# Performance work log

Hardware: AMD Instinct MI355X
Metric: run time of the kernel (lower is better)

## Reference

```python
import jax, jax.numpy as jnp
import numpy as np

DIM = 256
N_EMBED = 2048
EPS_LOG = 1e-07


def setup_inputs() -> dict:
    key = jax.random.key(0)
    k_in, k_emb = jax.random.split(key)
    inp = jax.random.normal(k_in, (16, 64, 64, DIM), dtype=jnp.float32)
    # embeddings_initial_variance = 1 -> plain randn
    embed = jax.random.normal(k_emb, (DIM, N_EMBED), dtype=jnp.float32)
    return {"input": inp, "embed": embed}


def reference(input, embed):
    # Eval-mode forward of Quantize (no EMA buffer updates).
    flatten = input.reshape(-1, DIM)                      # [N, dim]
    # squared euclidean distance via expansion:
    dist = (
        jnp.sum(flatten * flatten, axis=1, keepdims=True)
        - 2.0 * (flatten @ embed)
        + jnp.sum(embed * embed, axis=0, keepdims=True)
    )
    embed_ind_flat = jnp.argmax(-dist, axis=1)            # [N] int
    embed_ind = embed_ind_flat.reshape(input.shape[:-1])  # [B,H,W]

    # gather codes: F.embedding(embed_ind, embed.T)
    quantize = jnp.take(embed.T, embed_ind, axis=0)       # [B,H,W,dim]

    # commitment loss with detached quantize
    diff = jnp.mean((jax.lax.stop_gradient(quantize) - input) ** 2)

    # straight-through estimator
    quantize_st = input + jax.lax.stop_gradient(quantize - input)

    # perplexity from average code assignment probabilities
    n = flatten.shape[0]
    counts = jnp.zeros((N_EMBED,), dtype=flatten.dtype).at[embed_ind_flat].add(1.0)
    avg_probas = counts / n
    perplexity = jnp.exp(
        -jnp.sum(avg_probas * jnp.log(jnp.clip(avg_probas, EPS_LOG, None)))
    )
    return quantize_st, diff, embed_ind, perplexity
```

## Files before the change

### kernel.cpp

```cpp
#include <hip/hip_runtime.h>
#include <cstdint>
#include <cstddef>

#define DIM    256
#define NE     2048
#define NROWS  65536

#define OFF_DIFF ((size_t)16777216)
#define OFF_IND  ((size_t)16777217)
#define OFF_PERP ((size_t)16842753)

#define WS_DIFF   0
#define WS_CNT    64
#define WS_EN     8256
#define WS_ENC    16448
#define WS_ET     24640
#define WS_BPK    2121792
#define WS_NEED_V2 ((size_t)(2121792 + 2097152))

typedef __attribute__((ext_vector_type(8)))  _Float16 half8;
typedef __attribute__((ext_vector_type(16))) float    float16v;

__device__ __forceinline__ float16v mfma32(half8 a, half8 b, float16v c) {
    return __builtin_amdgcn_mfma_f32_32x32x16_f16(a, b, c, 0, 0, 0);
}

__device__ __forceinline__ void gld16(const void* g, void* l) {
    __builtin_amdgcn_global_load_lds((const __attribute__((address_space(1))) void*)g,
                                     (__attribute__((address_space(3))) void*)l,
                                     16, 0, 0);
}


__global__ __launch_bounds__(256) void k_prep(const float* __restrict__ embed,
                                              float* __restrict__ enorm,
                                              float* __restrict__ enc) {
    int j = blockIdx.x * 256 + threadIdx.x;
    double s = 0.0;
    for (int d = 0; d < DIM; ++d) {
        float e = embed[(size_t)d * NE + j];
        s += (double)e * (double)e;
    }
    float en = (float)s;
    enorm[j] = en;
    enc[j]   = (128.0f - 0.5f * en) * 2048.0f;
}

__global__ __launch_bounds__(256) void k_pack(const float* __restrict__ embed,
                                              _Float16* __restrict__ bpk,
                                              float* __restrict__ embedT) {
    int tt    = blockIdx.x * 256 + threadIdx.x;
    int nc    = tt >> 10;
    int tfrag = (tt >> 6) & 15;
    int lane  = tt & 63;
    int col   = nc * 32 + (lane & 31);
    int k0    = tfrag * 16 + (lane >> 5) * 8;
    half8 h, l;
#pragma unroll
    for (int j = 0; j < 8; ++j) {
        float e = embed[(size_t)(k0 + j) * NE + col];
        _Float16 eh = (_Float16)e;
        h[j] = eh;
        l[j] = (_Float16)(e - (float)eh);
        embedT[(size_t)col * DIM + k0 + j] = e;
    }
    char* base = (char*)bpk + (size_t)nc * 32768 + (size_t)tfrag * 1024 + (size_t)lane * 16;
    *(half8*)(base)         = h;
    *(half8*)(base + 16384) = l;
}


__global__ __launch_bounds__(256, 2) void k_gemm(
    const float* __restrict__ inp,
    const _Float16* __restrict__ bpk,
    const float* __restrict__ enorm,
    const float* __restrict__ enc,
    const float* __restrict__ embedT,
    float* __restrict__ out,
    int* __restrict__ counts,
    double* __restrict__ diffacc)
{
    __shared__ __align__(16) char ldsB[2][32768];
    __shared__ float encs[NE];
    const int tid  = threadIdx.x;
    const int w    = tid >> 6;
    const int lane = tid & 63;
    const int kh   = lane >> 5;
    const int m    = lane & 31;
    const int mw   = blockIdx.x * 128 + w * 32;

#pragma unroll
    for (int i = 0; i < 8; ++i) encs[tid + 256 * i] = enc[tid + 256 * i];

    half8 ah[16], al[16];
    {
        const float* xr = inp + (size_t)(mw + m) * DIM + kh * 8;
#pragma unroll
        for (int t = 0; t < 16; ++t) {
            float4 f0 = *(const float4*)(xr + t * 16);
            float4 f1 = *(const float4*)(xr + t * 16 + 4);
            float fs[8] = {f0.x, f0.y, f0.z, f0.w, f1.x, f1.y, f1.z, f1.w};
            half8 hh, ll;
#pragma unroll
            for (int j = 0; j < 8; ++j) {
                _Float16 xh = (_Float16)fs[j];
                hh[j] = xh;
                ll[j] = (_Float16)(fs[j] - (float)xh);
            }
            ah[t] = hh;
            al[t] = ll;
        }
    }

    int P1[16], P2[16];
#pragma unroll
    for (int r = 0; r < 16; ++r) { P1[r] = (int)0x80000000; P2[r] = (int)0x80000000; }

    {
        const char* src = (const char*)bpk;
#pragma unroll
        for (int s = 0; s < 8; ++s) {
            int seg = w * 8 + s;
            gld16(src + seg * 1024 + lane * 16, &ldsB[0][0] + seg * 1024);
        }
    }
    __syncthreads();

    for (int nc = 0; nc < 64; ++nc) {
        int pn = nc & 1;
        if (nc < 63) {
            const char* src = (const char*)bpk + (size_t)(nc + 1) * 32768;
            char* dst = &ldsB[pn ^ 1][0];
#pragma unroll
            for (int s = 0; s < 8; ++s) {
                int seg = w * 8 + s;
                gld16(src + seg * 1024 + lane * 16, dst + seg * 1024);
            }
        }

        float en = encs[nc * 32 + m];
        const char* bb = &ldsB[pn][0] + lane * 16;

        float16v acc = {};
#pragma unroll
        for (int t = 0; t < 16; ++t) {
            half8 bh = *(const half8*)(bb + t * 1024);
            half8 bl = *(const half8*)(bb + 16384 + t * 1024);
            acc = mfma32(ah[t], bh, acc);
            acc = mfma32(al[t], bh, acc);
            acc = mfma32(ah[t], bl, acc);
        }

        int colp = nc * 32 + m;
#pragma unroll
        for (int r = 0; r < 16; ++r) {
            float sf = fmaf(acc[r], 2048.0f, en);
            sf = __builtin_amdgcn_fmed3f(sf, -1048064.0f, 1048064.0f);
            int si = (int)sf;
            int p  = (int)(((unsigned)si << 11) | (unsigned)colp);
            int mn = (P1[r] < p) ? P1[r] : p;
            P2[r]  = (P2[r] > mn) ? P2[r] : mn;
            P1[r]  = (P1[r] > p) ? P1[r] : p;
        }
        __syncthreads();
    }

#pragma unroll
    for (int r = 0; r < 16; ++r) {
        int p1 = P1[r], p2 = P2[r];
#pragma unroll
        for (int msk = 1; msk < 32; msk <<= 1) {
            int o1 = __shfl_xor(p1, msk);
            int o2 = __shfl_xor(p2, msk);
            int mx2 = (p2 > o2) ? p2 : o2;
            int mn1 = (p1 < o1) ? p1 : o1;
            p2 = (mx2 > mn1) ? mx2 : mn1;
            p1 = (p1 > o1) ? p1 : o1;
        }
        P1[r] = p1; P2[r] = p2;
    }

    double dsum = 0.0;
#pragma unroll
    for (int rr = 0; rr < 32; ++rr) {
        const int reg = (rr & 3) | (((rr >> 3) & 3) << 2);
        const int src = ((rr >> 2) & 1) << 5;
        int i1 = __shfl(P1[reg], src) & 2047;
        int i2 = __shfl(P2[reg], src) & 2047;
        int row = mw + rr;
        float4 xv = *(const float4*)(inp    + (size_t)row * DIM + lane * 4);
        float4 e1 = *(const float4*)(embedT + (size_t)i1  * DIM + lane * 4);
        float4 e2 = *(const float4*)(embedT + (size_t)i2  * DIM + lane * 4);
        float d1 = xv.x * e1.x + xv.y * e1.y + xv.z * e1.z + xv.w * e1.w;
        float d2 = xv.x * e2.x + xv.y * e2.y + xv.z * e2.z + xv.w * e2.w;
#pragma unroll
        for (int msk = 1; msk < 64; msk <<= 1) {
            d1 += __shfl_xor(d1, msk);
            d2 += __shfl_xor(d2, msk);
        }
        float s1 = 2.f * d1 - enorm[i1];
        float s2 = 2.f * d2 - enorm[i2];
        bool take2 = (s2 > s1) || (s2 == s1 && i2 < i1);
        int win = take2 ? i2 : i1;
        float4 qv = take2 ? e2 : e1;
        *(float4*)(out + (size_t)row * DIM + lane * 4) = qv;
        float dx = qv.x - xv.x, dy = qv.y - xv.y;
        float dz = qv.z - xv.z, dw = qv.w - xv.w;
        dsum += (double)(dx * dx + dy * dy + dz * dz + dw * dw);
        if (lane == 0) {
            out[OFF_IND + row] = (float)win;
            atomicAdd(&counts[win], 1);
        }
    }
#pragma unroll
    for (int msk = 1; msk < 64; msk <<= 1) dsum += __shfl_xor(dsum, msk);
    if (lane == 0) atomicAdd(diffacc, dsum);
}

__global__ __launch_bounds__(256) void k_main(const float* __restrict__ inp,
                                              const float* __restrict__ embed,
                                              const float* __restrict__ enorm,
                                              float* __restrict__ out,
                                              int* __restrict__ counts,
                                              double* __restrict__ diffacc) {
    __shared__ float XsT[DIM][64];
    const int tid = threadIdx.x;
    const int m0  = blockIdx.x * 64;
#pragma unroll
    for (int i = 0; i < 16; ++i) {
        int f = tid + 256 * i;
        int row = f >> 6, c4 = f & 63;
        float4 v = *(const float4*)&inp[(size_t)(m0 + row) * DIM + c4 * 4];
        XsT[c4 * 4 + 0][row] = v.x; XsT[c4 * 4 + 1][row] = v.y;
        XsT[c4 * 4 + 2][row] = v.z; XsT[c4 * 4 + 3][row] = v.w;
    }
    __syncthreads();
    const int tx = tid & 15, ty = tid >> 4;
    float bv[4]; int bi[4];
#pragma unroll
    for (int mi = 0; mi < 4; ++mi) { bv[mi] = -1e30f; bi[mi] = 0x7fffffff; }
    for (int n0 = 0; n0 < NE; n0 += 64) {
        float acc[4][4] = {};
        const float* bp = embed + n0 + tx * 4;
        const float* ap = &XsT[0][ty * 4];
#pragma unroll 8
        for (int k = 0; k < DIM; ++k) {
            float4 b4 = *(const float4*)(bp + (size_t)k * NE);
            float4 a4 = *(const float4*)(ap + k * 64);
            acc[0][0] = fmaf(a4.x, b4.x, acc[0][0]); acc[0][1] = fmaf(a4.x, b4.y, acc[0][1]);
            acc[0][2] = fmaf(a4.x, b4.z, acc[0][2]); acc[0][3] = fmaf(a4.x, b4.w, acc[0][3]);
            acc[1][0] = fmaf(a4.y, b4.x, acc[1][0]); acc[1][1] = fmaf(a4.y, b4.y, acc[1][1]);
            acc[1][2] = fmaf(a4.y, b4.z, acc[1][2]); acc[1][3] = fmaf(a4.y, b4.w, acc[1][3]);
            acc[2][0] = fmaf(a4.z, b4.x, acc[2][0]); acc[2][1] = fmaf(a4.z, b4.y, acc[2][1]);
            acc[2][2] = fmaf(a4.z, b4.z, acc[2][2]); acc[2][3] = fmaf(a4.z, b4.w, acc[2][3]);
            acc[3][0] = fmaf(a4.w, b4.x, acc[3][0]); acc[3][1] = fmaf(a4.w, b4.y, acc[3][1]);
            acc[3][2] = fmaf(a4.w, b4.z, acc[3][2]); acc[3][3] = fmaf(a4.w, b4.w, acc[3][3]);
        }
        float4 en4 = *(const float4*)&enorm[n0 + tx * 4];
        int c0 = n0 + tx * 4;
#pragma unroll
        for (int mi = 0; mi < 4; ++mi) {
            float s0 = 2.f * acc[mi][0] - en4.x, s1 = 2.f * acc[mi][1] - en4.y;
            float s2 = 2.f * acc[mi][2] - en4.z, s3 = 2.f * acc[mi][3] - en4.w;
            float v = s0; int idx = c0;
            if (s1 > v) { v = s1; idx = c0 + 1; }
            if (s2 > v) { v = s2; idx = c0 + 2; }
            if (s3 > v) { v = s3; idx = c0 + 3; }
#pragma unroll
            for (int o = 1; o < 16; o <<= 1) {
                float ov = __shfl_xor(v, o, 64); int oi = __shfl_xor(idx, o, 64);
                if (ov > v || (ov == v && oi < idx)) { v = ov; idx = oi; }
            }
            if (v > bv[mi] || (v == bv[mi] && idx < bi[mi])) { bv[mi] = v; bi[mi] = idx; }
        }
    }
    __syncthreads();
    int* sidx = (int*)&XsT[0][0];
    if (tx == 0) {
#pragma unroll
        for (int mi = 0; mi < 4; ++mi) {
            int rl = ty * 4 + mi; int idx = bi[mi];
            sidx[rl] = idx;
            out[OFF_IND + m0 + rl] = (float)idx;
            atomicAdd(&counts[idx], 1);
        }
    }
    __syncthreads();
    float dsum = 0.f;
    for (int rl = 0; rl < 64; ++rl) {
        int idx = sidx[rl];
        float qv = embed[(size_t)tid * NE + idx];
        float x = inp[(size_t)(m0 + rl) * DIM + tid];
        out[(size_t)(m0 + rl) * DIM + tid] = qv;
        float d = qv - x;
        dsum = fmaf(d, d, dsum);
    }
    double ds = (double)dsum;
#pragma unroll
    for (int o = 32; o > 0; o >>= 1) ds += __shfl_down(ds, o, 64);
    double* red = (double*)&XsT[4][0];
    if ((tid & 63) == 0) red[tid >> 6] = ds;
    __syncthreads();
    if (tid == 0) atomicAdd(diffacc, red[0] + red[1] + red[2] + red[3]);
}

__global__ __launch_bounds__(256) void k_fin(const int* __restrict__ counts,
                                             const double* __restrict__ diffacc,
                                             float* __restrict__ out) {
    __shared__ double red[4];
    int tid = threadIdx.x;
    double s = 0.0;
    for (int i = tid; i < NE; i += 256) {
        int c = counts[i];
        if (c > 0) {
            float p = (float)c * (1.0f / 65536.0f);
            s += (double)(p * logf(p));
        }
    }
#pragma unroll
    for (int o = 32; o > 0; o >>= 1) s += __shfl_down(s, o, 64);
    if ((tid & 63) == 0) red[tid >> 6] = s;
    __syncthreads();
    if (tid == 0) {
        double t = red[0] + red[1] + red[2] + red[3];
        out[OFF_PERP] = expf((float)(-t));
        out[OFF_DIFF] = (float)(diffacc[0] * (1.0 / 16777216.0));
    }
}

extern "C" void kernel_launch(void* const* d_in, const int* in_sizes, int n_in,
                              void* d_out, int out_size, void* d_ws, size_t ws_size,
                              hipStream_t stream) {
    (void)in_sizes; (void)n_in; (void)out_size;
    const float* inp   = (const float*)d_in[0];
    const float* embed = (const float*)d_in[1];
    float* out = (float*)d_out;
    char*  ws  = (char*)d_ws;

    double*   diffacc = (double*)(ws + WS_DIFF);
    int*      counts  = (int*)(ws + WS_CNT);
    float*    enorm   = (float*)(ws + WS_EN);
    float*    enc     = (float*)(ws + WS_ENC);
    float*    embedT  = (float*)(ws + WS_ET);
    _Float16* bpk     = (_Float16*)(ws + WS_BPK);

    hipMemsetAsync(d_ws, 0, 8256, stream);
    k_prep<<<NE / 256, 256, 0, stream>>>(embed, enorm, enc);

    if (ws_size >= WS_NEED_V2) {
        k_pack<<<256, 256, 0, stream>>>(embed, bpk, embedT);
        k_gemm<<<NROWS / 128, 256, 0, stream>>>(inp, bpk, enorm, enc, embedT,
                                                out, counts, diffacc);
    } else {
        k_main<<<NROWS / 64, 256, 0, stream>>>(inp, embed, enorm,
                                               out, counts, diffacc);
    }
    k_fin<<<1, 256, 0, stream>>>(counts, diffacc, out);
}
```

Measured before the change: 335.3 us.

## Drop low-half embedding term, flag near-tie rows and recheck them in fp32

```diff
diff --git a/kernel.cpp b/kernel.cpp
--- a/kernel.cpp
+++ b/kernel.cpp
@@ -11,12 +11,13 @@
 #define OFF_PERP ((size_t)16842753)
 
 #define WS_DIFF   0
+#define WS_NFLAG  8
 #define WS_CNT    64
 #define WS_EN     8256
-#define WS_ENC    16448
-#define WS_ET     24640
-#define WS_BPK    2121792
-#define WS_NEED_V2 ((size_t)(2121792 + 2097152))
+#define WS_FLAG   16448
+#define WS_ET     32832
+#define WS_BPH    2129984
+#define FLAG_CAP  4096
 
 typedef __attribute__((ext_vector_type(8)))  _Float16 half8;
 typedef __attribute__((ext_vector_type(16))) float    float16v;
@@ -31,23 +32,30 @@
                                      16, 0, 0);
 }
 
-
 __global__ __launch_bounds__(256) void k_prep(const float* __restrict__ embed,
-                                              float* __restrict__ enorm,
-                                              float* __restrict__ enc) {
-    int j = blockIdx.x * 256 + threadIdx.x;
+                                              float* __restrict__ enorm) {
+    __shared__ double red[256];
+    const int tid = threadIdx.x;
+    const int cl  = tid & 31, seg = tid >> 5;
+    const int col = blockIdx.x * 32 + cl;
     double s = 0.0;
-    for (int d = 0; d < DIM; ++d) {
-        float e = embed[(size_t)d * NE + j];
+#pragma unroll 8
+    for (int k = seg * 32; k < seg * 32 + 32; ++k) {
+        float e = embed[(size_t)k * NE + col];
         s += (double)e * (double)e;
     }
-    float en = (float)s;
-    enorm[j] = en;
-    enc[j]   = (128.0f - 0.5f * en) * 2048.0f;
+    red[tid] = s;
+    __syncthreads();
+    if (seg == 0) {
+        double t = 0.0;
+#pragma unroll
+        for (int h = 0; h < 8; ++h) t += red[cl + 32 * h];
+        enorm[col] = (float)t;
+    }
 }
 
 __global__ __launch_bounds__(256) void k_pack(const float* __restrict__ embed,
-                                              _Float16* __restrict__ bpk,
+                                              _Float16* __restrict__ bph,
                                               float* __restrict__ embedT) {
     int tt    = blockIdx.x * 256 + threadIdx.x;
     int nc    = tt >> 10;
@@ -55,46 +63,37 @@
     int lane  = tt & 63;
     int col   = nc * 32 + (lane & 31);
     int k0    = tfrag * 16 + (lane >> 5) * 8;
-    half8 h, l;
+    half8 h;
 #pragma unroll
     for (int j = 0; j < 8; ++j) {
         float e = embed[(size_t)(k0 + j) * NE + col];
-        _Float16 eh = (_Float16)e;
-        h[j] = eh;
-        l[j] = (_Float16)(e - (float)eh);
+        h[j] = (_Float16)e;
         embedT[(size_t)col * DIM + k0 + j] = e;
     }
-    char* base = (char*)bpk + (size_t)nc * 32768 + (size_t)tfrag * 1024 + (size_t)lane * 16;
-    *(half8*)(base)         = h;
-    *(half8*)(base + 16384) = l;
-}
-
+    *(half8*)((char*)bph + (size_t)nc * 16384 + (size_t)tfrag * 1024 + (size_t)lane * 16) = h;
+}
 
 __global__ __launch_bounds__(256, 2) void k_gemm(
     const float* __restrict__ inp,
-    const _Float16* __restrict__ bpk,
+    const _Float16* __restrict__ bph,
     const float* __restrict__ enorm,
-    const float* __restrict__ enc,
     const float* __restrict__ embedT,
     float* __restrict__ out,
     int* __restrict__ counts,
-    double* __restrict__ diffacc)
+    double* __restrict__ diffacc,
+    int* __restrict__ nflag,
+    int* __restrict__ flags)
 {
-    __shared__ __align__(16) char ldsB[2][32768];
-    __shared__ float encs[NE];
+    __shared__ __align__(16) char ldsB[2][16384];
     const int tid  = threadIdx.x;
     const int w    = tid >> 6;
     const int lane = tid & 63;
-    const int kh   = lane >> 5;
     const int m    = lane & 31;
     const int mw   = blockIdx.x * 128 + w * 32;
 
-#pragma unroll
-    for (int i = 0; i < 8; ++i) encs[tid + 256 * i] = enc[tid + 256 * i];
-
     half8 ah[16], al[16];
     {
-        const float* xr = inp + (size_t)(mw + m) * DIM + kh * 8;
+        const float* xr = inp + (size_t)(mw + m) * DIM + (lane >> 5) * 8;
 #pragma unroll
         for (int t = 0; t < 16; ++t) {
             float4 f0 = *(const float4*)(xr + t * 16);
@@ -116,45 +115,40 @@
 #pragma unroll
     for (int r = 0; r < 16; ++r) { P1[r] = (int)0x80000000; P2[r] = (int)0x80000000; }
 
-    {
-        const char* src = (const char*)bpk;
-#pragma unroll
-        for (int s = 0; s < 8; ++s) {
-            int seg = w * 8 + s;
-            gld16(src + seg * 1024 + lane * 16, &ldsB[0][0] + seg * 1024);
-        }
+#pragma unroll
+    for (int s = 0; s < 4; ++s) {
+        int seg = w * 4 + s;
+        gld16((const char*)bph + seg * 1024 + lane * 16, &ldsB[0][0] + seg * 1024);
     }
     __syncthreads();
 
     for (int nc = 0; nc < 64; ++nc) {
         int pn = nc & 1;
         if (nc < 63) {
-            const char* src = (const char*)bpk + (size_t)(nc + 1) * 32768;
+            const char* src = (const char*)bph + (size_t)(nc + 1) * 16384;
             char* dst = &ldsB[pn ^ 1][0];
 #pragma unroll
-            for (int s = 0; s < 8; ++s) {
-                int seg = w * 8 + s;
+            for (int s = 0; s < 4; ++s) {
+                int seg = w * 4 + s;
                 gld16(src + seg * 1024 + lane * 16, dst + seg * 1024);
             }
         }
 
-        float en = encs[nc * 32 + m];
         const char* bb = &ldsB[pn][0] + lane * 16;
-
-        float16v acc = {};
+        float16v accA = {}, accB = {};
 #pragma unroll
         for (int t = 0; t < 16; ++t) {
             half8 bh = *(const half8*)(bb + t * 1024);
-            half8 bl = *(const half8*)(bb + 16384 + t * 1024);
-            acc = mfma32(ah[t], bh, acc);
-            acc = mfma32(al[t], bh, acc);
-            acc = mfma32(ah[t], bl, acc);
-        }
-
-        int colp = nc * 32 + m;
+            accA = mfma32(ah[t], bh, accA);
+            accB = mfma32(al[t], bh, accB);
+        }
+
+        float en  = enorm[nc * 32 + m];
+        float enc = fmaf(en, -1024.0f, 262144.0f);
+        int colp  = nc * 32 + m;
 #pragma unroll
         for (int r = 0; r < 16; ++r) {
-            float sf = fmaf(acc[r], 2048.0f, en);
+            float sf = fmaf(accA[r] + accB[r], 2048.0f, enc);
             sf = __builtin_amdgcn_fmed3f(sf, -1048064.0f, 1048064.0f);
             int si = (int)sf;
             int p  = (int)(((unsigned)si << 11) | (unsigned)colp);
@@ -185,8 +179,11 @@
     for (int rr = 0; rr < 32; ++rr) {
         const int reg = (rr & 3) | (((rr >> 3) & 3) << 2);
         const int src = ((rr >> 2) & 1) << 5;
-        int i1 = __shfl(P1[reg], src) & 2047;
-        int i2 = __shfl(P2[reg], src) & 2047;
+        int p1row = __shfl(P1[reg], src);
+        int p2row = __shfl(P2[reg], src);
+        int i1 = p1row & 2047;
+        int i2 = p2row & 2047;
+        float v2a = (float)(p2row >> 11) * (1.0f / 1024.0f) - 256.0f;
         int row = mw + rr;
         float4 xv = *(const float4*)(inp    + (size_t)row * DIM + lane * 4);
         float4 e1 = *(const float4*)(embedT + (size_t)i1  * DIM + lane * 4);
@@ -202,6 +199,7 @@
         float s2 = 2.f * d2 - enorm[i2];
         bool take2 = (s2 > s1) || (s2 == s1 && i2 < i1);
         int win = take2 ? i2 : i1;
+        float sW = take2 ? s2 : s1;
         float4 qv = take2 ? e2 : e1;
         *(float4*)(out + (size_t)row * DIM + lane * 4) = qv;
         float dx = qv.x - xv.x, dy = qv.y - xv.y;
@@ -210,6 +208,10 @@
         if (lane == 0) {
             out[OFF_IND + row] = (float)win;
             atomicAdd(&counts[win], 1);
+            if (sW - v2a < 0.15f) {
+                int fi = atomicAdd(nflag, 1);
+                if (fi < FLAG_CAP) flags[fi] = row;
+            }
         }
     }
 #pragma unroll
@@ -217,91 +219,119 @@
     if (lane == 0) atomicAdd(diffacc, dsum);
 }
 
-__global__ __launch_bounds__(256) void k_main(const float* __restrict__ inp,
-                                              const float* __restrict__ embed,
-                                              const float* __restrict__ enorm,
-                                              float* __restrict__ out,
-                                              int* __restrict__ counts,
-                                              double* __restrict__ diffacc) {
+__global__ __launch_bounds__(256) void k_clean(
+    const float* __restrict__ inp,
+    const float* __restrict__ embed,
+    const float* __restrict__ embedT,
+    const float* __restrict__ enorm,
+    float* __restrict__ out,
+    int* __restrict__ counts,
+    double* __restrict__ diffacc,
+    const int* __restrict__ nflagp,
+    const int* __restrict__ flags)
+{
     __shared__ float XsT[DIM][64];
+    __shared__ int rowsS[64];
+    __shared__ int newS[64];
+    __shared__ double redS[4];
+    int nf = *nflagp; if (nf > FLAG_CAP) nf = FLAG_CAP;
     const int tid = threadIdx.x;
-    const int m0  = blockIdx.x * 64;
-#pragma unroll
-    for (int i = 0; i < 16; ++i) {
-        int f = tid + 256 * i;
-        int row = f >> 6, c4 = f & 63;
-        float4 v = *(const float4*)&inp[(size_t)(m0 + row) * DIM + c4 * 4];
-        XsT[c4 * 4 + 0][row] = v.x; XsT[c4 * 4 + 1][row] = v.y;
-        XsT[c4 * 4 + 2][row] = v.z; XsT[c4 * 4 + 3][row] = v.w;
-    }
-    __syncthreads();
-    const int tx = tid & 15, ty = tid >> 4;
-    float bv[4]; int bi[4];
-#pragma unroll
-    for (int mi = 0; mi < 4; ++mi) { bv[mi] = -1e30f; bi[mi] = 0x7fffffff; }
-    for (int n0 = 0; n0 < NE; n0 += 64) {
-        float acc[4][4] = {};
-        const float* bp = embed + n0 + tx * 4;
-        const float* ap = &XsT[0][ty * 4];
+
+    for (int chunk = blockIdx.x; chunk * 64 < nf; chunk += gridDim.x) {
+        int cnt = nf - chunk * 64; if (cnt > 64) cnt = 64;
+        if (tid < 64) {
+            rowsS[tid] = flags[chunk * 64 + (tid < cnt ? tid : 0)];
+            newS[tid] = -1;
+        }
+        __syncthreads();
+#pragma unroll
+        for (int i = 0; i < 16; ++i) {
+            int f = tid + 256 * i;
+            int r = f >> 6, c4 = f & 63;
+            float4 v = *(const float4*)&inp[(size_t)rowsS[r] * DIM + c4 * 4];
+            XsT[c4 * 4 + 0][r] = v.x; XsT[c4 * 4 + 1][r] = v.y;
+            XsT[c4 * 4 + 2][r] = v.z; XsT[c4 * 4 + 3][r] = v.w;
+        }
+        __syncthreads();
+
+        const int tx = tid & 15, ty = tid >> 4;
+        float bv[4]; int bi[4];
+#pragma unroll
+        for (int mi = 0; mi < 4; ++mi) { bv[mi] = -1e30f; bi[mi] = 0x7fffffff; }
+        for (int n0 = 0; n0 < NE; n0 += 64) {
+            float acc[4][4] = {};
+            const float* bp = embed + n0 + tx * 4;
+            const float* ap = &XsT[0][ty * 4];
 #pragma unroll 8
-        for (int k = 0; k < DIM; ++k) {
-            float4 b4 = *(const float4*)(bp + (size_t)k * NE);
-            float4 a4 = *(const float4*)(ap + k * 64);
-            acc[0][0] = fmaf(a4.x, b4.x, acc[0][0]); acc[0][1] = fmaf(a4.x, b4.y, acc[0][1]);
-            acc[0][2] = fmaf(a4.x, b4.z, acc[0][2]); acc[0][3] = fmaf(a4.x, b4.w, acc[0][3]);
-            acc[1][0] = fmaf(a4.y, b4.x, acc[1][0]); acc[1][1] = fmaf(a4.y, b4.y, acc[1][1]);
-            acc[1][2] = fmaf(a4.y, b4.z, acc[1][2]); acc[1][3] = fmaf(a4.y, b4.w, acc[1][3]);
-            acc[2][0] = fmaf(a4.z, b4.x, acc[2][0]); acc[2][1] = fmaf(a4.z, b4.y, acc[2][1]);
-            acc[2][2] = fmaf(a4.z, b4.z, acc[2][2]); acc[2][3] = fmaf(a4.z, b4.w, acc[2][3]);
-            acc[3][0] = fmaf(a4.w, b4.x, acc[3][0]); acc[3][1] = fmaf(a4.w, b4.y, acc[3][1]);
-            acc[3][2] = fmaf(a4.w, b4.z, acc[3][2]); acc[3][3] = fmaf(a4.w, b4.w, acc[3][3]);
-        }
-        float4 en4 = *(const float4*)&enorm[n0 + tx * 4];
-        int c0 = n0 + tx * 4;
-#pragma unroll
-        for (int mi = 0; mi < 4; ++mi) {
-            float s0 = 2.f * acc[mi][0] - en4.x, s1 = 2.f * acc[mi][1] - en4.y;
-            float s2 = 2.f * acc[mi][2] - en4.z, s3 = 2.f * acc[mi][3] - en4.w;
-            float v = s0; int idx = c0;
-            if (s1 > v) { v = s1; idx = c0 + 1; }
-            if (s2 > v) { v = s2; idx = c0 + 2; }
-            if (s3 > v) { v = s3; idx = c0 + 3; }
-#pragma unroll
-            for (int o = 1; o < 16; o <<= 1) {
-                float ov = __shfl_xor(v, o, 64); int oi = __shfl_xor(idx, o, 64);
-                if (ov > v || (ov == v && oi < idx)) { v = ov; idx = oi; }
-            }
-            if (v > bv[mi] || (v == bv[mi] && idx < bi[mi])) { bv[mi] = v; bi[mi] = idx; }
-        }
-    }
-    __syncthreads();
-    int* sidx = (int*)&XsT[0][0];
-    if (tx == 0) {
-#pragma unroll
-        for (int mi = 0; mi < 4; ++mi) {
-            int rl = ty * 4 + mi; int idx = bi[mi];
-            sidx[rl] = idx;
-            out[OFF_IND + m0 + rl] = (float)idx;
-            atomicAdd(&counts[idx], 1);
-        }
-    }
-    __syncthreads();
-    float dsum = 0.f;
-    for (int rl = 0; rl < 64; ++rl) {
-        int idx = sidx[rl];
-        float qv = embed[(size_t)tid * NE + idx];
-        float x = inp[(size_t)(m0 + rl) * DIM + tid];
-        out[(size_t)(m0 + rl) * DIM + tid] = qv;
-        float d = qv - x;
-        dsum = fmaf(d, d, dsum);
-    }
-    double ds = (double)dsum;
-#pragma unroll
-    for (int o = 32; o > 0; o >>= 1) ds += __shfl_down(ds, o, 64);
-    double* red = (double*)&XsT[4][0];
-    if ((tid & 63) == 0) red[tid >> 6] = ds;
-    __syncthreads();
-    if (tid == 0) atomicAdd(diffacc, red[0] + red[1] + red[2] + red[3]);
+            for (int k = 0; k < DIM; ++k) {
+                float4 b4 = *(const float4*)(bp + (size_t)k * NE);
+                float4 a4 = *(const float4*)(ap + k * 64);
+                acc[0][0] = fmaf(a4.x, b4.x, acc[0][0]); acc[0][1] = fmaf(a4.x, b4.y, acc[0][1]);
+                acc[0][2] = fmaf(a4.x, b4.z, acc[0][2]); acc[0][3] = fmaf(a4.x, b4.w, acc[0][3]);
+                acc[1][0] = fmaf(a4.y, b4.x, acc[1][0]); acc[1][1] = fmaf(a4.y, b4.y, acc[1][1]);
+                acc[1][2] = fmaf(a4.y, b4.z, acc[1][2]); acc[1][3] = fmaf(a4.y, b4.w, acc[1][3]);
+                acc[2][0] = fmaf(a4.z, b4.x, acc[2][0]); acc[2][1] = fmaf(a4.z, b4.y, acc[2][1]);
+                acc[2][2] = fmaf(a4.z, b4.z, acc[2][2]); acc[2][3] = fmaf(a4.z, b4.w, acc[2][3]);
+                acc[3][0] = fmaf(a4.w, b4.x, acc[3][0]); acc[3][1] = fmaf(a4.w, b4.y, acc[3][1]);
+                acc[3][2] = fmaf(a4.w, b4.z, acc[3][2]); acc[3][3] = fmaf(a4.w, b4.w, acc[3][3]);
+            }
+            float4 en4 = *(const float4*)&enorm[n0 + tx * 4];
+            int c0 = n0 + tx * 4;
+#pragma unroll
+            for (int mi = 0; mi < 4; ++mi) {
+                float s0 = 2.f * acc[mi][0] - en4.x, s1 = 2.f * acc[mi][1] - en4.y;
+                float s2 = 2.f * acc[mi][2] - en4.z, s3 = 2.f * acc[mi][3] - en4.w;
+                float v = s0; int idx = c0;
+                if (s1 > v) { v = s1; idx = c0 + 1; }
+                if (s2 > v) { v = s2; idx = c0 + 2; }
+                if (s3 > v) { v = s3; idx = c0 + 3; }
+#pragma unroll
+                for (int o = 1; o < 16; o <<= 1) {
+                    float ov = __shfl_xor(v, o, 64); int oi = __shfl_xor(idx, o, 64);
+                    if (ov > v || (ov == v && oi < idx)) { v = ov; idx = oi; }
+                }
+                if (v > bv[mi] || (v == bv[mi] && idx < bi[mi])) { bv[mi] = v; bi[mi] = idx; }
+            }
+        }
+        if (tx == 0) {
+#pragma unroll
+            for (int mi = 0; mi < 4; ++mi) {
+                int rl = ty * 4 + mi;
+                if (rl < cnt) {
+                    int row  = rowsS[rl];
+                    int oldw = (int)out[OFF_IND + row];
+                    if (bi[mi] != oldw) newS[rl] = bi[mi];
+                }
+            }
+        }
+        __syncthreads();
+
+        for (int r = 0; r < 64; ++r) {
+            int nw = newS[r];
+            if (nw < 0) continue;
+            int row  = rowsS[r];
+            int oldw = (int)out[OFF_IND + row];
+            float x   = XsT[tid][r];
+            float env = embedT[(size_t)nw   * DIM + tid];
+            float eov = embedT[(size_t)oldw * DIM + tid];
+            out[(size_t)row * DIM + tid] = env;
+            float dn = env - x;
+            float dov = eov - x;
+            double d = (double)(dn * dn) - (double)(dov * dov);
+#pragma unroll
+            for (int msk = 1; msk < 64; msk <<= 1) d += __shfl_xor(d, msk);
+            if ((tid & 63) == 0) redS[tid >> 6] = d;
+            __syncthreads();
+            if (tid == 0) {
+                atomicAdd(diffacc, redS[0] + redS[1] + redS[2] + redS[3]);
+                atomicAdd(&counts[oldw], -1);
+                atomicAdd(&counts[nw], 1);
+                out[OFF_IND + row] = (float)nw;
+            }
+            __syncthreads();
+        }
+        __syncthreads();
+    }
 }
 
 __global__ __launch_bounds__(256) void k_fin(const int* __restrict__ counts,
@@ -331,29 +361,26 @@
 extern "C" void kernel_launch(void* const* d_in, const int* in_sizes, int n_in,
                               void* d_out, int out_size, void* d_ws, size_t ws_size,
                               hipStream_t stream) {
-    (void)in_sizes; (void)n_in; (void)out_size;
+    (void)in_sizes; (void)n_in; (void)out_size; (void)ws_size;
     const float* inp   = (const float*)d_in[0];
     const float* embed = (const float*)d_in[1];
     float* out = (float*)d_out;
     char*  ws  = (char*)d_ws;
 
     double*   diffacc = (double*)(ws + WS_DIFF);
+    int*      nflag   = (int*)(ws + WS_NFLAG);
     int*      counts  = (int*)(ws + WS_CNT);
     float*    enorm   = (float*)(ws + WS_EN);
-    float*    enc     = (float*)(ws + WS_ENC);
+    int*      flags   = (int*)(ws + WS_FLAG);
     float*    embedT  = (float*)(ws + WS_ET);
-    _Float16* bpk     = (_Float16*)(ws + WS_BPK);
-
-    hipMemsetAsync(d_ws, 0, 8256, stream);
-    k_prep<<<NE / 256, 256, 0, stream>>>(embed, enorm, enc);
-
-    if (ws_size >= WS_NEED_V2) {
-        k_pack<<<256, 256, 0, stream>>>(embed, bpk, embedT);
-        k_gemm<<<NROWS / 128, 256, 0, stream>>>(inp, bpk, enorm, enc, embedT,
-                                                out, counts, diffacc);
-    } else {
-        k_main<<<NROWS / 64, 256, 0, stream>>>(inp, embed, enorm,
-                                               out, counts, diffacc);
-    }
+    _Float16* bph     = (_Float16*)(ws + WS_BPH);
+
+    (void)hipMemsetAsync(d_ws, 0, 8256, stream);
+    k_prep<<<NE / 32, 256, 0, stream>>>(embed, enorm);
+    k_pack<<<256, 256, 0, stream>>>(embed, bph, embedT);
+    k_gemm<<<NROWS / 128, 256, 0, stream>>>(inp, bph, enorm, embedT,
+                                            out, counts, diffacc, nflag, flags);
+    k_clean<<<64, 256, 0, stream>>>(inp, embed, embedT, enorm,
+                                    out, counts, diffacc, nflag, flags);
     k_fin<<<1, 256, 0, stream>>>(counts, diffacc, out);
 }
```

After: 829.0 us. 147% more time.
